# Kernel optimization log

Hardware: AMD Instinct MI355X
Metric: run time of the kernel (lower is better)

The kernel has to match this reference:

```python
import jax, jax.numpy as jnp
import numpy as np

N_NODES = 100000  # size_u + size_v + size_w
N_MP = 3          # metapaths vv, uu, ww
N_EDGES = 1000000
D_IN = 64
D_OUT = 64


def setup_inputs() -> dict:
    key = jax.random.key(0)
    k1, k2, k3, k4 = jax.random.split(key, 4)
    x = jax.random.normal(k1, (N_NODES, D_IN), dtype=jnp.float32)
    # per-metapath GCNConv weight (glorot-ish scale)
    W = jax.random.normal(k2, (N_MP, D_IN, D_OUT), dtype=jnp.float32) * (1.0 / np.sqrt(D_IN))
    edge_index = jax.random.randint(k3, (N_MP, 2, N_EDGES), 0, N_NODES, dtype=jnp.int64)
    edge_weight = jax.random.uniform(k4, (N_MP, N_EDGES), dtype=jnp.float32)
    return {"x": x, "W": W, "edge_index": edge_index, "edge_weight": edge_weight}


def _gcn_conv(x, w_mat, row, col, ew, num_nodes):
    # gcn_norm without self-loops: deg[i] = sum of edge weights into i
    deg = jax.ops.segment_sum(ew, col, num_segments=num_nodes)
    dinv = jnp.where(deg > 0, jax.lax.rsqrt(jnp.where(deg > 0, deg, 1.0)), 0.0)
    norm = dinv[row] * ew * dinv[col]          # [E]
    h = x @ w_mat                               # [N, D_OUT]
    msg = h[row] * norm[:, None]                # [E, D_OUT] gather + scale
    return jax.ops.segment_sum(msg, col, num_segments=num_nodes)  # scatter-add


def reference(x, W, edge_index, edge_weight):
    num_nodes = x.shape[0]
    outs = []
    for i in range(N_MP):  # small fixed loop over structurally distinct encoders
        row = edge_index[i, 0]
        col = edge_index[i, 1]
        out = _gcn_conv(x, W[i], row, col, edge_weight[i], num_nodes)
        outs.append(jax.nn.relu(out))  # act=nn.ReLU
    return jnp.stack(outs)  # [3, N, D_OUT]; dropout omitted (eval mode)
```

## Files before the change

### kernel.cpp

```cpp
#include <hip/hip_runtime.h>
#include <hip/hip_fp16.h>

#define NNODES 100000
#define NMP 3
#define NEDGES 1000000
#define D 64
#define NTOT (NMP * NNODES)
#define BINW 1024
#define NBIN 293
#define CAPB 10944
#define T1 5632
#define RPT 11
#define OVCAP 131072

typedef __attribute__((ext_vector_type(8))) short bf16x8;
typedef __attribute__((ext_vector_type(4))) float floatx4;

__device__ __forceinline__ unsigned short f2bf(float f) {
    unsigned u = __float_as_uint(f);
    u = (u + 0x7FFFu + ((u >> 16) & 1u)) >> 16;
    return (unsigned short)u;
}
__device__ __forceinline__ __half2 u2h(unsigned u) {
    __half2 r;
    *reinterpret_cast<unsigned*>(&r) = u;
    return r;
}

__global__ __launch_bounds__(512) void split_kernel(const int* __restrict__ ei,
                                                    const float* __restrict__ ew,
                                                    int* __restrict__ gcur,
                                                    int* __restrict__ ovcur,
                                                    int* __restrict__ ovf,
                                                    uint2* __restrict__ A) {
    __shared__ uint2 stage[T1];
    __shared__ unsigned short sbin[T1];
    __shared__ int hist[NBIN], lbase[NBIN], gbase[NBIN], lcur[NBIN];
    __shared__ int sh[512];
    const int t = threadIdx.x;
    const int mp = blockIdx.y;
    const int e0 = blockIdx.x * T1;
    const int nrec = min(T1, NEDGES - e0);
    for (int i = t; i < NBIN; i += 512) hist[i] = 0;
    __syncthreads();
    unsigned key[RPT]; float w[RPT]; int bn[RPT];
#pragma unroll
    for (int i = 0; i < RPT; ++i) {
        int e = e0 + i * 512 + t;
        bn[i] = -1;
        if (e < NEDGES) {
            int r = ei[(mp * 2 + 0) * NEDGES + e];
            int c = ei[(mp * 2 + 1) * NEDGES + e];
            w[i] = ew[mp * NEDGES + e];
            int cflat = mp * NNODES + c;
            int rflat = mp * NNODES + r;
            int b = cflat >> 10;
            bn[i] = b;
            key[i] = ((unsigned)(cflat & 1023) << 19) | (unsigned)rflat;
            atomicAdd(&hist[b], 1);
        }
    }
    __syncthreads();
    int v = (t < NBIN) ? hist[t] : 0;
    sh[t] = v;
    __syncthreads();
    for (int d = 1; d < 512; d <<= 1) {
        int add = (t >= d) ? sh[t - d] : 0;
        __syncthreads();
        sh[t] += add;
        __syncthreads();
    }
    if (t < NBIN) {
        int ex = sh[t] - v;
        lbase[t] = ex;
        lcur[t] = ex;
        gbase[t] = v ? atomicAdd(&gcur[t], v) : 0;
    }
    __syncthreads();
#pragma unroll
    for (int i = 0; i < RPT; ++i) {
        if (bn[i] >= 0) {
            int s = atomicAdd(&lcur[bn[i]], 1);
            stage[s] = make_uint2(key[i], __float_as_uint(w[i]));
            sbin[s] = (unsigned short)bn[i];
        }
    }
    __syncthreads();
    for (int s = t; s < nrec; s += 512) {
        int b = sbin[s];
        uint2 rec = stage[s];
        int pos = gbase[b] + (s - lbase[b]);
        if (pos < CAPB) {
            A[(size_t)b * CAPB + pos] = rec;
        } else {
            int op = atomicAdd(ovcur, 1);
            if (op < OVCAP) {
                int cflat = (b << 10) | (int)(rec.x >> 19);
                ovf[3 * op] = cflat;
                ovf[3 * op + 1] = (int)(rec.x & 0x7FFFFu);
                ovf[3 * op + 2] = (int)rec.y;
            }
        }
    }
}

__global__ __launch_bounds__(256) void compact2_kernel(const int* __restrict__ gcur,
                                                       const uint2* __restrict__ A,
                                                       const int* __restrict__ ovcur,
                                                       const int* __restrict__ ovf,
                                                       uint2* __restrict__ C,
                                                       int2* __restrict__ nodeoff,
                                                       float* __restrict__ dinv) {
    const int bin = blockIdx.x;
    __shared__ int cnt[BINW];
    __shared__ float wsum[BINW];
    __shared__ int pos[BINW];
    __shared__ int sh[256];
    const int t = threadIdx.x;
    for (int i = t; i < BINW; i += 256) { cnt[i] = 0; wsum[i] = 0.0f; }
    __syncthreads();
    const int len = min(gcur[bin], CAPB);
    const uint2* Ab = A + (size_t)bin * CAPB;
    for (int p = t; p < len; p += 256) {
        uint2 rec = Ab[p];
        atomicAdd(&cnt[rec.x >> 19], 1);
        atomicAdd(&wsum[rec.x >> 19], __uint_as_float(rec.y));
    }
    const int ovn = min(*ovcur, OVCAP);
    for (int i = t; i < ovn; i += 256) {
        int cflat = ovf[3 * i];
        if ((cflat >> 10) == bin) {
            atomicAdd(&cnt[cflat & 1023], 1);
            atomicAdd(&wsum[cflat & 1023], __int_as_float(ovf[3 * i + 2]));
        }
    }
    __syncthreads();
    int c0 = cnt[4 * t], c1 = cnt[4 * t + 1], c2 = cnt[4 * t + 2], c3 = cnt[4 * t + 3];
    int vsum = c0 + c1 + c2 + c3;
    sh[t] = vsum;
    __syncthreads();
    for (int d = 1; d < 256; d <<= 1) {
        int add = (t >= d) ? sh[t - d] : 0;
        __syncthreads();
        sh[t] += add;
        __syncthreads();
    }
    const int base = bin * CAPB;
    const int lim = base + CAPB;
    int p0 = base + sh[t] - vsum;
    int p1 = p0 + c0, p2 = p1 + c1, p3 = p2 + c2;
    pos[4 * t] = p0; pos[4 * t + 1] = p1; pos[4 * t + 2] = p2; pos[4 * t + 3] = p3;
    int starts[4] = {p0, p1, p2, p3};
    int cs[4] = {c0, c1, c2, c3};
#pragma unroll
    for (int j = 0; j < 4; ++j) {
        int cl = 4 * t + j;
        int node = (bin << 10) + cl;
        if (node < NTOT) {
            nodeoff[node] = make_int2(starts[j], cs[j]);
            float dg = wsum[cl];
            dinv[node] = (dg > 0.0f) ? rsqrtf(dg) : 0.0f;
        }
    }
    __syncthreads();
    for (int p = t; p < len; p += 256) {
        uint2 rec = Ab[p];
        int s = atomicAdd(&pos[rec.x >> 19], 1);
        if (s < lim) C[s] = make_uint2(rec.x & 0x7FFFFu, rec.y);
    }
    for (int i = t; i < ovn; i += 256) {
        int cflat = ovf[3 * i];
        if ((cflat >> 10) == bin) {
            int s = atomicAdd(&pos[cflat & 1023], 1);
            if (s < lim) C[s] = make_uint2((unsigned)ovf[3 * i + 1], (unsigned)ovf[3 * i + 2]);
        }
    }
}

__global__ __launch_bounds__(256) void prep_w_kernel(const float* __restrict__ W,
                                                     unsigned short* __restrict__ wT) {
    int idx = blockIdx.x * 256 + threadIdx.x;
    if (idx >= NMP * D * D) return;
    int mp = idx >> 12, rem = idx & 4095;
    int k = rem >> 6, n = rem & 63;
    wT[(mp * D + n) * D + k] = f2bf(W[idx]);
}

__global__ __launch_bounds__(256) void gemm_kernel(const float* __restrict__ x,
                                                   const unsigned short* __restrict__ wT,
                                                   const float* __restrict__ dinv,
                                                   unsigned short* __restrict__ h) {
    const int wave = threadIdx.x >> 6;
    const int lane = threadIdx.x & 63;
    const int rowbase = (blockIdx.x * 4 + wave) * 16;
    if (rowbase >= NNODES) return;
    const int m = lane & 15;
    const int q = lane >> 4;
    const float4* xr = (const float4*)(x + (size_t)(rowbase + m) * D);
    bf16x8 a[2];
#pragma unroll
    for (int kc = 0; kc < 2; ++kc) {
        float4 x0 = xr[kc * 8 + q * 2];
        float4 x1 = xr[kc * 8 + q * 2 + 1];
        a[kc][0] = f2bf(x0.x); a[kc][1] = f2bf(x0.y);
        a[kc][2] = f2bf(x0.z); a[kc][3] = f2bf(x0.w);
        a[kc][4] = f2bf(x1.x); a[kc][5] = f2bf(x1.y);
        a[kc][6] = f2bf(x1.z); a[kc][7] = f2bf(x1.w);
    }
#pragma unroll
    for (int mp = 0; mp < NMP; ++mp) {
        float dv = dinv[mp * NNODES + rowbase + m];
#pragma unroll
        for (int nt = 0; nt < 4; ++nt) {
            const bf16x8* bp = (const bf16x8*)(wT + (size_t)(mp * D + nt * 16 + m) * D);
            bf16x8 b0 = bp[q];
            bf16x8 b1 = bp[4 + q];
            floatx4 acc = {0.f, 0.f, 0.f, 0.f};
            acc = __builtin_amdgcn_mfma_f32_16x16x32_bf16(b0, a[0], acc, 0, 0, 0);
            acc = __builtin_amdgcn_mfma_f32_16x16x32_bf16(b1, a[1], acc, 0, 0, 0);
            unsigned v0 = (unsigned)__half_as_ushort(__float2half(acc[0] * dv)) |
                          ((unsigned)__half_as_ushort(__float2half(acc[1] * dv)) << 16);
            unsigned v1 = (unsigned)__half_as_ushort(__float2half(acc[2] * dv)) |
                          ((unsigned)__half_as_ushort(__float2half(acc[3] * dv)) << 16);
            *(uint2*)(h + ((size_t)mp * NNODES + rowbase + m) * D + nt * 16 + q * 4) =
                make_uint2(v0, v1);
        }
    }
}

__global__ __launch_bounds__(256) void gather_kernel(const int2* __restrict__ nodeoff,
                                                     const uint2* __restrict__ dense,
                                                     const unsigned short* __restrict__ h,
                                                     const float* __restrict__ dinv,
                                                     float* __restrict__ out) {
    const int tid = threadIdx.x;
    const int wave = tid >> 6, lane = tid & 63;
    const int sub = lane >> 5;
    const int g = (lane >> 3) & 3;
    const int f = lane & 7;
    const int w = blockIdx.x * 8 + wave * 2 + sub;
    int2 off = nodeoff[w];
    const int start = off.x, end = off.x + off.y;
    const uint4* hp = (const uint4*)h;
    __half2 acc2[4];
    acc2[0] = __float2half2_rn(0.0f); acc2[1] = __float2half2_rn(0.0f);
    acc2[2] = __float2half2_rn(0.0f); acc2[3] = __float2half2_rn(0.0f);
    if (end > start) {
        const int last = end - 1;
        uint2 prA = dense[min(start + g, last)];
        uint2 prB = dense[min(start + 4 + g, last)];
        uint4 hvA = hp[(size_t)prA.x * 8 + f];
        for (int p = start; p < end; p += 4) {
            uint2 prC = dense[min(p + 8 + g, last)];
            uint4 hvB = hp[(size_t)prB.x * 8 + f];
            float wgt = (p + g < end) ? __uint_as_float(prA.y) : 0.0f;
            __half2 wp = __float2half2_rn(wgt);
            acc2[0] = __hfma2(u2h(hvA.x), wp, acc2[0]);
            acc2[1] = __hfma2(u2h(hvA.y), wp, acc2[1]);
            acc2[2] = __hfma2(u2h(hvA.z), wp, acc2[2]);
            acc2[3] = __hfma2(u2h(hvA.w), wp, acc2[3]);
            prA = prB; hvA = hvB; prB = prC;
        }
    }
    float acc[8];
    acc[0] = __low2float(acc2[0]); acc[1] = __high2float(acc2[0]);
    acc[2] = __low2float(acc2[1]); acc[3] = __high2float(acc2[1]);
    acc[4] = __low2float(acc2[2]); acc[5] = __high2float(acc2[2]);
    acc[6] = __low2float(acc2[3]); acc[7] = __high2float(acc2[3]);
#pragma unroll
    for (int j = 0; j < 8; ++j) {
        acc[j] += __shfl_xor(acc[j], 8);
        acc[j] += __shfl_xor(acc[j], 16);
    }
    float dv = dinv[w];
    if (g < 2) {
        float4 o = g ? make_float4(acc[4], acc[5], acc[6], acc[7])
                     : make_float4(acc[0], acc[1], acc[2], acc[3]);
        o.x = fmaxf(o.x * dv, 0.0f);
        o.y = fmaxf(o.y * dv, 0.0f);
        o.z = fmaxf(o.z * dv, 0.0f);
        o.w = fmaxf(o.w * dv, 0.0f);
        ((float4*)out)[(size_t)w * 16 + f * 2 + g] = o;
    }
}

extern "C" void kernel_launch(void* const* d_in, const int* in_sizes, int n_in,
                              void* d_out, int out_size, void* d_ws, size_t ws_size,
                              hipStream_t stream) {
    const float* x  = (const float*)d_in[0];
    const float* W  = (const float*)d_in[1];
    const int*   ei = (const int*)d_in[2];
    const float* ew = (const float*)d_in[3];
    float* out = (float*)d_out;

    char* ws = (char*)d_ws;
    uint2* A           = (uint2*)(ws + 0);
    unsigned short* h  = (unsigned short*)(ws + 0);
    uint2* C           = (uint2*)(ws + 38400000);
    int2*  nodeoff     = (int2*)(ws + 64052736);
    float* dinv        = (float*)(ws + 66452736);
    unsigned short* wT = (unsigned short*)(ws + 67652736);
    int*   gcur        = (int*)(ws + 67677312);
    int*   ovcur       = (int*)(ws + 67678484);
    int*   ovf         = (int*)(ws + 67678488);

    hipMemsetAsync(gcur, 0, 1176, stream);

    split_kernel<<<dim3((NEDGES + T1 - 1) / T1, NMP), 512, 0, stream>>>(ei, ew, gcur,
                                                                        ovcur, ovf, A);
    compact2_kernel<<<NBIN, 256, 0, stream>>>(gcur, A, ovcur, ovf, C, nodeoff, dinv);
    prep_w_kernel<<<(NMP * D * D + 255) / 256, 256, 0, stream>>>(W, wT);
    gemm_kernel<<<(NNODES / 16 + 3) / 4, 256, 0, stream>>>(x, wT, dinv, h);
    gather_kernel<<<NTOT / 8, 256, 0, stream>>>(nodeoff, C, h, dinv, out);
}
```

Baseline: 285.6 us.

## Fuse per-bin CSR compaction into gather via shared-memory permutation

Removes the global compacted edge array and node offset table. Each bin is now handled by two blocks, each covering half of the feature columns. A block rebuilds per-node counts and a local permutation in shared memory, then gathers h rows straight from the bin-partitioned buffer, and a lighter deg kernel computes only dinv. This saves the global write and re-read of the compacted edges. In exchange, the two blocks per bin duplicate the counting and sorting work, Ab is read indirectly through perm, and each output node now scans the whole overflow list serially.

Result: slower. 404.2 us (+41.5%).

```diff
diff --git a/kernel.cpp b/kernel.cpp
--- a/kernel.cpp
+++ b/kernel.cpp
@@ -25,6 +25,12 @@
     __half2 r;
     *reinterpret_cast<unsigned*>(&r) = u;
     return r;
+}
+__device__ __forceinline__ float h2f_lo(unsigned u) {
+    return __half2float(__ushort_as_half((unsigned short)(u & 0xFFFFu)));
+}
+__device__ __forceinline__ float h2f_hi(unsigned u) {
+    return __half2float(__ushort_as_half((unsigned short)(u >> 16)));
 }
 
 __global__ __launch_bounds__(512) void split_kernel(const int* __restrict__ ei,
@@ -104,75 +110,34 @@
     }
 }
 
-__global__ __launch_bounds__(256) void compact2_kernel(const int* __restrict__ gcur,
-                                                       const uint2* __restrict__ A,
-                                                       const int* __restrict__ ovcur,
-                                                       const int* __restrict__ ovf,
-                                                       uint2* __restrict__ C,
-                                                       int2* __restrict__ nodeoff,
-                                                       float* __restrict__ dinv) {
+__global__ __launch_bounds__(256) void deg_kernel(const int* __restrict__ gcur,
+                                                  const uint2* __restrict__ A,
+                                                  const int* __restrict__ ovcur,
+                                                  const int* __restrict__ ovf,
+                                                  float* __restrict__ dinv) {
     const int bin = blockIdx.x;
-    __shared__ int cnt[BINW];
     __shared__ float wsum[BINW];
-    __shared__ int pos[BINW];
-    __shared__ int sh[256];
     const int t = threadIdx.x;
-    for (int i = t; i < BINW; i += 256) { cnt[i] = 0; wsum[i] = 0.0f; }
+    for (int i = t; i < BINW; i += 256) wsum[i] = 0.0f;
     __syncthreads();
     const int len = min(gcur[bin], CAPB);
     const uint2* Ab = A + (size_t)bin * CAPB;
     for (int p = t; p < len; p += 256) {
         uint2 rec = Ab[p];
-        atomicAdd(&cnt[rec.x >> 19], 1);
         atomicAdd(&wsum[rec.x >> 19], __uint_as_float(rec.y));
     }
     const int ovn = min(*ovcur, OVCAP);
     for (int i = t; i < ovn; i += 256) {
         int cflat = ovf[3 * i];
-        if ((cflat >> 10) == bin) {
-            atomicAdd(&cnt[cflat & 1023], 1);
+        if ((cflat >> 10) == bin)
             atomicAdd(&wsum[cflat & 1023], __int_as_float(ovf[3 * i + 2]));
-        }
-    }
-    __syncthreads();
-    int c0 = cnt[4 * t], c1 = cnt[4 * t + 1], c2 = cnt[4 * t + 2], c3 = cnt[4 * t + 3];
-    int vsum = c0 + c1 + c2 + c3;
-    sh[t] = vsum;
-    __syncthreads();
-    for (int d = 1; d < 256; d <<= 1) {
-        int add = (t >= d) ? sh[t - d] : 0;
-        __syncthreads();
-        sh[t] += add;
-        __syncthreads();
-    }
-    const int base = bin * CAPB;
-    const int lim = base + CAPB;
-    int p0 = base + sh[t] - vsum;
-    int p1 = p0 + c0, p2 = p1 + c1, p3 = p2 + c2;
-    pos[4 * t] = p0; pos[4 * t + 1] = p1; pos[4 * t + 2] = p2; pos[4 * t + 3] = p3;
-    int starts[4] = {p0, p1, p2, p3};
-    int cs[4] = {c0, c1, c2, c3};
-#pragma unroll
-    for (int j = 0; j < 4; ++j) {
-        int cl = 4 * t + j;
-        int node = (bin << 10) + cl;
-        if (node < NTOT) {
-            nodeoff[node] = make_int2(starts[j], cs[j]);
-            float dg = wsum[cl];
-            dinv[node] = (dg > 0.0f) ? rsqrtf(dg) : 0.0f;
-        }
-    }
-    __syncthreads();
-    for (int p = t; p < len; p += 256) {
-        uint2 rec = Ab[p];
-        int s = atomicAdd(&pos[rec.x >> 19], 1);
-        if (s < lim) C[s] = make_uint2(rec.x & 0x7FFFFu, rec.y);
-    }
-    for (int i = t; i < ovn; i += 256) {
-        int cflat = ovf[3 * i];
-        if ((cflat >> 10) == bin) {
-            int s = atomicAdd(&pos[cflat & 1023], 1);
-            if (s < lim) C[s] = make_uint2((unsigned)ovf[3 * i + 1], (unsigned)ovf[3 * i + 2]);
+    }
+    __syncthreads();
+    for (int n = t; n < BINW; n += 256) {
+        int nf = (bin << 10) + n;
+        if (nf < NTOT) {
+            float dg = wsum[n];
+            dinv[nf] = (dg > 0.0f) ? rsqrtf(dg) : 0.0f;
         }
     }
 }
@@ -228,59 +193,110 @@
     }
 }
 
-__global__ __launch_bounds__(256) void gather_kernel(const int2* __restrict__ nodeoff,
-                                                     const uint2* __restrict__ dense,
-                                                     const unsigned short* __restrict__ h,
-                                                     const float* __restrict__ dinv,
-                                                     float* __restrict__ out) {
-    const int tid = threadIdx.x;
-    const int wave = tid >> 6, lane = tid & 63;
+__global__ __launch_bounds__(512) void bin_gather_kernel(const int* __restrict__ gcur,
+                                                         const uint2* __restrict__ A,
+                                                         const int* __restrict__ ovcur,
+                                                         const int* __restrict__ ovf,
+                                                         const unsigned short* __restrict__ h,
+                                                         const float* __restrict__ dinv,
+                                                         float* __restrict__ out) {
+    const int bin = blockIdx.x >> 1;
+    const int fh = blockIdx.x & 1;
+    __shared__ int cnt[BINW];
+    __shared__ int nstart[BINW];
+    __shared__ int pcur[BINW];
+    __shared__ int sh[512];
+    __shared__ unsigned short perm[CAPB];
+    const int t = threadIdx.x;
+    for (int i = t; i < BINW; i += 512) cnt[i] = 0;
+    __syncthreads();
+    const int len = min(gcur[bin], CAPB);
+    const uint2* Ab = A + (size_t)bin * CAPB;
+    for (int s = t; s < len; s += 512) atomicAdd(&cnt[Ab[s].x >> 19], 1);
+    __syncthreads();
+    int c0 = cnt[2 * t], c1 = cnt[2 * t + 1];
+    int v = c0 + c1;
+    sh[t] = v;
+    __syncthreads();
+    for (int d = 1; d < 512; d <<= 1) {
+        int add = (t >= d) ? sh[t - d] : 0;
+        __syncthreads();
+        sh[t] += add;
+        __syncthreads();
+    }
+    int ex = sh[t] - v;
+    nstart[2 * t] = ex;      nstart[2 * t + 1] = ex + c0;
+    pcur[2 * t] = ex;        pcur[2 * t + 1] = ex + c0;
+    __syncthreads();
+    for (int s = t; s < len; s += 512) {
+        int slot = atomicAdd(&pcur[Ab[s].x >> 19], 1);
+        perm[slot] = (unsigned short)s;
+    }
+    __syncthreads();
+    const int wave = t >> 6, lane = t & 63;
     const int sub = lane >> 5;
-    const int g = (lane >> 3) & 3;
-    const int f = lane & 7;
-    const int w = blockIdx.x * 8 + wave * 2 + sub;
-    int2 off = nodeoff[w];
-    const int start = off.x, end = off.x + off.y;
+    const int g = (lane >> 2) & 7;
+    const int f = lane & 3;
+    const int hsel = fh * 4 + f;
     const uint4* hp = (const uint4*)h;
-    __half2 acc2[4];
-    acc2[0] = __float2half2_rn(0.0f); acc2[1] = __float2half2_rn(0.0f);
-    acc2[2] = __float2half2_rn(0.0f); acc2[3] = __float2half2_rn(0.0f);
-    if (end > start) {
-        const int last = end - 1;
-        uint2 prA = dense[min(start + g, last)];
-        uint2 prB = dense[min(start + 4 + g, last)];
-        uint4 hvA = hp[(size_t)prA.x * 8 + f];
-        for (int p = start; p < end; p += 4) {
-            uint2 prC = dense[min(p + 8 + g, last)];
-            uint4 hvB = hp[(size_t)prB.x * 8 + f];
-            float wgt = (p + g < end) ? __uint_as_float(prA.y) : 0.0f;
-            __half2 wp = __float2half2_rn(wgt);
-            acc2[0] = __hfma2(u2h(hvA.x), wp, acc2[0]);
-            acc2[1] = __hfma2(u2h(hvA.y), wp, acc2[1]);
-            acc2[2] = __hfma2(u2h(hvA.z), wp, acc2[2]);
-            acc2[3] = __hfma2(u2h(hvA.w), wp, acc2[3]);
-            prA = prB; hvA = hvB; prB = prC;
-        }
-    }
-    float acc[8];
-    acc[0] = __low2float(acc2[0]); acc[1] = __high2float(acc2[0]);
-    acc[2] = __low2float(acc2[1]); acc[3] = __high2float(acc2[1]);
-    acc[4] = __low2float(acc2[2]); acc[5] = __high2float(acc2[2]);
-    acc[6] = __low2float(acc2[3]); acc[7] = __high2float(acc2[3]);
-#pragma unroll
-    for (int j = 0; j < 8; ++j) {
-        acc[j] += __shfl_xor(acc[j], 8);
-        acc[j] += __shfl_xor(acc[j], 16);
-    }
-    float dv = dinv[w];
-    if (g < 2) {
-        float4 o = g ? make_float4(acc[4], acc[5], acc[6], acc[7])
-                     : make_float4(acc[0], acc[1], acc[2], acc[3]);
-        o.x = fmaxf(o.x * dv, 0.0f);
-        o.y = fmaxf(o.y * dv, 0.0f);
-        o.z = fmaxf(o.z * dv, 0.0f);
-        o.w = fmaxf(o.w * dv, 0.0f);
-        ((float4*)out)[(size_t)w * 16 + f * 2 + g] = o;
+    const int ovn = min(*ovcur, OVCAP);
+    for (int rnd = 0; rnd < BINW / 16; ++rnd) {
+        const int nl = rnd * 16 + wave * 2 + sub;
+        const int n = (bin << 10) + nl;
+        if (n >= NTOT) continue;
+        const int start = nstart[nl];
+        const int end = start + cnt[nl];
+        __half2 acc2[4];
+        acc2[0] = __float2half2_rn(0.0f); acc2[1] = __float2half2_rn(0.0f);
+        acc2[2] = __float2half2_rn(0.0f); acc2[3] = __float2half2_rn(0.0f);
+        if (end > start) {
+            const int last = end - 1;
+            uint2 rA = Ab[perm[min(start + g, last)]];
+            uint2 rB = Ab[perm[min(start + 8 + g, last)]];
+            uint4 hA = hp[(size_t)(rA.x & 0x7FFFFu) * 8 + hsel];
+            for (int p = start; p < end; p += 8) {
+                uint2 rC = Ab[perm[min(p + 16 + g, last)]];
+                uint4 hB = hp[(size_t)(rB.x & 0x7FFFFu) * 8 + hsel];
+                float wgt = (p + g < end) ? __uint_as_float(rA.y) : 0.0f;
+                __half2 wp = __float2half2_rn(wgt);
+                acc2[0] = __hfma2(u2h(hA.x), wp, acc2[0]);
+                acc2[1] = __hfma2(u2h(hA.y), wp, acc2[1]);
+                acc2[2] = __hfma2(u2h(hA.z), wp, acc2[2]);
+                acc2[3] = __hfma2(u2h(hA.w), wp, acc2[3]);
+                rA = rB; hA = hB; rB = rC;
+            }
+        }
+        float acc[8];
+        acc[0] = __low2float(acc2[0]); acc[1] = __high2float(acc2[0]);
+        acc[2] = __low2float(acc2[1]); acc[3] = __high2float(acc2[1]);
+        acc[4] = __low2float(acc2[2]); acc[5] = __high2float(acc2[2]);
+        acc[6] = __low2float(acc2[3]); acc[7] = __high2float(acc2[3]);
+#pragma unroll
+        for (int j = 0; j < 8; ++j) {
+            acc[j] += __shfl_xor(acc[j], 4);
+            acc[j] += __shfl_xor(acc[j], 8);
+            acc[j] += __shfl_xor(acc[j], 16);
+        }
+        if (g < 2) {
+            for (int i = 0; i < ovn; ++i) {
+                if (ovf[3 * i] == n) {
+                    float wgt = __int_as_float(ovf[3 * i + 2]);
+                    uint4 hv = hp[(size_t)ovf[3 * i + 1] * 8 + hsel];
+                    acc[0] += wgt * h2f_lo(hv.x); acc[1] += wgt * h2f_hi(hv.x);
+                    acc[2] += wgt * h2f_lo(hv.y); acc[3] += wgt * h2f_hi(hv.y);
+                    acc[4] += wgt * h2f_lo(hv.z); acc[5] += wgt * h2f_hi(hv.z);
+                    acc[6] += wgt * h2f_lo(hv.w); acc[7] += wgt * h2f_hi(hv.w);
+                }
+            }
+            float dv = dinv[n];
+            float4 o = g ? make_float4(acc[4], acc[5], acc[6], acc[7])
+                         : make_float4(acc[0], acc[1], acc[2], acc[3]);
+            o.x = fmaxf(o.x * dv, 0.0f);
+            o.y = fmaxf(o.y * dv, 0.0f);
+            o.z = fmaxf(o.z * dv, 0.0f);
+            o.w = fmaxf(o.w * dv, 0.0f);
+            ((float4*)out)[(size_t)n * 16 + fh * 8 + f * 2 + g] = o;
+        }
     }
 }
 
@@ -295,21 +311,19 @@
 
     char* ws = (char*)d_ws;
     uint2* A           = (uint2*)(ws + 0);
-    unsigned short* h  = (unsigned short*)(ws + 0);
-    uint2* C           = (uint2*)(ws + 38400000);
-    int2*  nodeoff     = (int2*)(ws + 64052736);
-    float* dinv        = (float*)(ws + 66452736);
-    unsigned short* wT = (unsigned short*)(ws + 67652736);
-    int*   gcur        = (int*)(ws + 67677312);
-    int*   ovcur       = (int*)(ws + 67678484);
-    int*   ovf         = (int*)(ws + 67678488);
+    unsigned short* h  = (unsigned short*)(ws + 25652736);
+    float* dinv        = (float*)(ws + 64052736);
+    unsigned short* wT = (unsigned short*)(ws + 65252736);
+    int*   gcur        = (int*)(ws + 65277312);
+    int*   ovcur       = (int*)(ws + 65278484);
+    int*   ovf         = (int*)(ws + 65278488);
 
     hipMemsetAsync(gcur, 0, 1176, stream);
 
     split_kernel<<<dim3((NEDGES + T1 - 1) / T1, NMP), 512, 0, stream>>>(ei, ew, gcur,
                                                                         ovcur, ovf, A);
-    compact2_kernel<<<NBIN, 256, 0, stream>>>(gcur, A, ovcur, ovf, C, nodeoff, dinv);
+    deg_kernel<<<NBIN, 256, 0, stream>>>(gcur, A, ovcur, ovf, dinv);
     prep_w_kernel<<<(NMP * D * D + 255) / 256, 256, 0, stream>>>(W, wT);
     gemm_kernel<<<(NNODES / 16 + 3) / 4, 256, 0, stream>>>(x, wT, dinv, h);
-    gather_kernel<<<NTOT / 8, 256, 0, stream>>>(nodeoff, C, h, dinv, out);
-}
+    bin_gather_kernel<<<NBIN * 2, 512, 0, stream>>>(gcur, A, ovcur, ovf, h, dinv, out);
+}
```
